# Performance work log

Measured on AMD Instinct MI355X. Metric: run time of the kernel, lower is better.

Reference implementation:

```python
import jax, jax.numpy as jnp
import numpy as np

T, B, E, H = 2048, 4, 1024, 16
D = E // H  # head_dim = 64
SCALING = D ** -0.5


def setup_inputs() -> dict:
    key = jax.random.key(0)
    ks = jax.random.split(key, 5)
    w_scale = (2.0 / (E + E)) ** 0.5  # xavier_uniform-ish std
    return {
        "query": jax.random.normal(ks[0], (T, B, E), dtype=jnp.float32),
        "q_weight": jax.random.normal(ks[1], (E, E), dtype=jnp.float32) * w_scale,
        "k_weight": jax.random.normal(ks[2], (E, E), dtype=jnp.float32) * w_scale,
        "v_weight": jax.random.normal(ks[3], (E, E), dtype=jnp.float32) * w_scale,
        "out_proj_weight": jax.random.normal(ks[4], (E, E), dtype=jnp.float32) * w_scale,
        "q_bias": jnp.zeros((E,), dtype=jnp.float32),
        "k_bias": jnp.zeros((E,), dtype=jnp.float32),
        "v_bias": jnp.zeros((E,), dtype=jnp.float32),
        "out_proj_bias": jnp.zeros((E,), dtype=jnp.float32),
    }


def reference(query, q_weight, k_weight, v_weight, out_proj_weight,
              q_bias, k_bias, v_bias, out_proj_bias):
    # Linear projections: y = x @ W.T + b  (torch F.linear convention)
    q = jnp.einsum('tbe,fe->tbf', query, q_weight) + q_bias
    k = jnp.einsum('tbe,fe->tbf', query, k_weight) + k_bias
    v = jnp.einsum('tbe,fe->tbf', query, v_weight) + v_bias
    # split heads: [T, B, H, D]
    q = q.reshape(T, B, H, D) * SCALING
    k = k.reshape(T, B, H, D)
    v = v.reshape(T, B, H, D)
    # attention scores [B, H, T, T] over keys s
    scores = jnp.einsum('tbhd,sbhd->bhts', q, k)
    attn = jax.nn.softmax(scores, axis=-1)
    # context [T, B, H, D] -> [T, B, E]
    ctx = jnp.einsum('bhts,sbhd->tbhd', attn, v).reshape(T, B, E)
    # output projection
    out = jnp.einsum('tbe,fe->tbf', ctx, out_proj_weight) + out_proj_bias
    return out
```

## Files before the change

kernel.cpp:

```cpp
#include <hip/hip_runtime.h>
#include <hip/hip_bf16.h>
#include <stdint.h>

#define T_   2048
#define B_   4
#define E_   1024
#define H_   16
#define D_   64
#define M_   8192
#define KDIM 1024

using bf16 = __hip_bfloat16;
typedef __attribute__((ext_vector_type(8)))  short bf16x8;
typedef __attribute__((ext_vector_type(4)))  float f32x4;
typedef __attribute__((ext_vector_type(16))) float f32x16;

#define QK_SCALE 0.180336880f

#if __has_builtin(__builtin_amdgcn_exp2f)
#define EXP2F(x) __builtin_amdgcn_exp2f(x)
#else
#define EXP2F(x) exp2f(x)
#endif

__device__ __forceinline__ void gload_lds16(const void* g, void* l) {
  __builtin_amdgcn_global_load_lds(
      (const __attribute__((address_space(1))) void*)g,
      (__attribute__((address_space(3))) void*)l, 16, 0, 0);
}

__device__ __forceinline__ uint32_t pack_bf16(float lo, float hi) {
  union { __hip_bfloat162 h2; uint32_t u; } cv;
  cv.h2 = __float22bfloat162_rn(float2{lo, hi});
  return cv.u;
}

__device__ __forceinline__ void plswap(uint32_t& a, uint32_t& b) {
#if __has_builtin(__builtin_amdgcn_permlane32_swap)
  typedef __attribute__((ext_vector_type(2))) unsigned int u32x2_t;
  u32x2_t r = __builtin_amdgcn_permlane32_swap(a, b, false, false);
  a = r[0]; b = r[1];
#else
  asm volatile("v_permlane32_swap_b32 %0, %1" : "+v"(a), "+v"(b));
#endif
}
__device__ __forceinline__ float comb_add32(float x) {
  union { float f; uint32_t u; } a, b; a.f = x; b.f = x;
  plswap(a.u, b.u);
  return a.f + b.f;
}

__global__ void k_cvt_all(const float* __restrict__ X,
                          const float* __restrict__ Wq, const float* __restrict__ Wk,
                          const float* __restrict__ Wv, const float* __restrict__ Wo,
                          bf16* __restrict__ Xb,
                          bf16* __restrict__ Wqb, bf16* __restrict__ Wkb,
                          bf16* __restrict__ Wvb, bf16* __restrict__ Wob) {
  int id = blockIdx.x;
  const float* src; bf16* dst; int base;
  if (id < 8192) { src = X; dst = Xb; base = id; }
  else {
    int w = (id - 8192) >> 10;
    base = (id - 8192) & 1023;
    src = (w == 0) ? Wq : (w == 1) ? Wk : (w == 2) ? Wv : Wo;
    dst = (w == 0) ? Wqb : (w == 1) ? Wkb : (w == 2) ? Wvb : Wob;
  }
  int i = base * 256 + threadIdx.x;
  float4 v = reinterpret_cast<const float4*>(src)[i];
  bf16* d = dst + (size_t)i * 4;
  d[0] = __float2bfloat16(v.x);
  d[1] = __float2bfloat16(v.y);
  d[2] = __float2bfloat16(v.z);
  d[3] = __float2bfloat16(v.w);
}

__device__ __forceinline__ void gemm_tile_body(
    const bf16* __restrict__ A, const bf16* __restrict__ Bw,
    int bm, int bn, bf16* sA, bf16* sB, f32x4 (&acc)[4][4])
{
  const int t    = threadIdx.x;
  const int wave = t >> 6;
  const int lane = t & 63;
  const int l15  = lane & 15, l4 = lane >> 4;
  const int wr = wave >> 1, wc = wave & 1;
  const int srow = t >> 3;
  const int sg   = t & 7;

  for (int k0 = 0; k0 < KDIM; k0 += 64) {
#pragma unroll
    for (int rd = 0; rd < 4; ++rd) {
      int row = rd * 32 + srow;
      const bf16* src = A + (size_t)(bm * 128 + row) * KDIM + k0 + ((sg ^ (row & 7)) * 8);
      gload_lds16(src, sA + rd * 2048 + wave * 512);
    }
#pragma unroll
    for (int rd = 0; rd < 4; ++rd) {
      int row = rd * 32 + srow;
      const bf16* src = Bw + (size_t)(bn * 128 + row) * KDIM + k0 + ((sg ^ (row & 7)) * 8);
      gload_lds16(src, sB + rd * 2048 + wave * 512);
    }
    __syncthreads();

#pragma unroll
    for (int kk = 0; kk < 2; ++kk) {
      bf16x8 af[4], bfr[4];
#pragma unroll
      for (int m = 0; m < 4; ++m) {
        int row = wr * 64 + m * 16 + l15;
        int ch  = (l4 + kk * 4) ^ (row & 7);
        af[m] = *(const bf16x8*)(sA + row * 64 + ch * 8);
      }
#pragma unroll
      for (int n = 0; n < 4; ++n) {
        int row = wc * 64 + n * 16 + l15;
        int ch  = (l4 + kk * 4) ^ (row & 7);
        bfr[n] = *(const bf16x8*)(sB + row * 64 + ch * 8);
      }
#pragma unroll
      for (int m = 0; m < 4; ++m)
#pragma unroll
        for (int n = 0; n < 4; ++n)
          acc[m][n] = __builtin_amdgcn_mfma_f32_16x16x32_bf16(af[m], bfr[n], acc[m][n], 0, 0, 0);
    }
    __syncthreads();
  }
}

__global__ __launch_bounds__(256, 3) void k_gemm_qkv(
    const bf16* __restrict__ A,
    const bf16* __restrict__ Wq, const bf16* __restrict__ Wk, const bf16* __restrict__ Wv,
    const float* __restrict__ bq, const float* __restrict__ bk, const float* __restrict__ bv,
    bf16* __restrict__ outQ)
{
  __shared__ bf16 sA[128 * 64];
  __shared__ bf16 sB[128 * 64];
  const int bid = blockIdx.x;
  const int xcd = bid & 7;
  const int l   = bid >> 3;
  const int g   = l / 24;
  const int w   = l % 24;
  const int bm  = g * 8 + (w & 7);
  const int bn  = xcd * 3 + (w >> 3);
  const int which = bn >> 3;
  const int bnn = bn & 7;
  const bf16* Bw = (which == 0) ? Wq : (which == 1) ? Wk : Wv;
  const float* bias = (which == 0) ? bq : (which == 1) ? bk : bv;
  const float scale = (which == 0) ? QK_SCALE : 1.0f;
  bf16* outb = outQ + (size_t)which * M_ * E_;

  f32x4 acc[4][4] = {};
  gemm_tile_body(A, Bw, bm, bnn, sA, sB, acc);

  const int lane = threadIdx.x & 63;
  const int l15 = lane & 15, l4 = lane >> 4;
  const int wave = threadIdx.x >> 6;
  const int wr = wave >> 1, wc = wave & 1;
#pragma unroll
  for (int m = 0; m < 4; ++m) {
#pragma unroll
    for (int n = 0; n < 4; ++n) {
      int gc = bnn * 128 + wc * 64 + n * 16 + l15;
      float bv_ = bias[gc];
#pragma unroll
      for (int r = 0; r < 4; ++r) {
        int gr = bm * 128 + wr * 64 + m * 16 + l4 * 4 + r;
        float v = (acc[m][n][r] + bv_) * scale;
        int tt = gr >> 2, bb = gr & 3;
        int hh = gc >> 6, dd = gc & 63;
        outb[(((size_t)(bb * H_ + hh)) * T_ + tt) * D_ + dd] = __float2bfloat16(v);
      }
    }
  }
}

__global__ __launch_bounds__(256, 3) void k_gemm_out(
    const bf16* __restrict__ A, const bf16* __restrict__ Bw,
    const float* __restrict__ bias, float* __restrict__ outf)
{
  __shared__ bf16 sA[128 * 64];
  __shared__ bf16 sB[128 * 64];
  const int bid = blockIdx.x;
  const int swz = (bid & 7) * 64 + (bid >> 3);
  const int bm = swz & 63;
  const int bn = swz >> 6;

  f32x4 acc[4][4] = {};
  gemm_tile_body(A, Bw, bm, bn, sA, sB, acc);

  const int lane = threadIdx.x & 63;
  const int l15 = lane & 15, l4 = lane >> 4;
  const int wave = threadIdx.x >> 6;
  const int wr = wave >> 1, wc = wave & 1;
#pragma unroll
  for (int m = 0; m < 4; ++m) {
#pragma unroll
    for (int n = 0; n < 4; ++n) {
      int gc = bn * 128 + wc * 64 + n * 16 + l15;
      float bv_ = bias[gc];
#pragma unroll
      for (int r = 0; r < 4; ++r) {
        int gr = bm * 128 + wr * 64 + m * 16 + l4 * 4 + r;
        outf[(size_t)gr * E_ + gc] = acc[m][n][r] + bv_;
      }
    }
  }
}

__global__ __launch_bounds__(256, 4) void k_attn5(
    const bf16* __restrict__ Qb, const bf16* __restrict__ Kb,
    const bf16* __restrict__ Vb, bf16* __restrict__ ctx)
{
  __shared__ bf16 sK [128 * 64];
  __shared__ bf16 sVT[2 * 64 * 64];

  const int t    = threadIdx.x;
  const int wave = t >> 6;
  const int lane = t & 63;
  const int l31  = lane & 31;
  const int h    = lane >> 5;

  const int bid = blockIdx.x;
  const int swz = (bid & 7) * 128 + (bid >> 3);
  const int bh  = swz >> 4;
  const int qt  = swz & 15;
  const int q0  = qt * 128;
  const size_t headoff = (size_t)bh * T_ * D_;

  const int qrow = q0 + wave * 32 + l31;
  bf16x8 qf[4];
#pragma unroll
  for (int kc = 0; kc < 4; ++kc)
    qf[kc] = *(const bf16x8*)(Qb + headoff + (size_t)qrow * 64 + kc * 16 + 8 * h);

  f32x16 acc0 = {}, acc1 = {};
  float lrun = 0.f;

  const int srow = t >> 3, sg = t & 7;
  const int vkey = (t >> 3) * 2, vd0 = (t & 7) * 8;

  int off_qk[4][2];
#pragma unroll
  for (int kc = 0; kc < 4; ++kc) {
    int slot = ((2 * kc + h) ^ (l31 & 7)) * 8;
    off_qk[kc][0] = l31 * 64 + slot;
    off_qk[kc][1] = (32 + l31) * 64 + slot;
  }
  int off_pv[4][2];
#pragma unroll
  for (int ks = 0; ks < 4; ++ks) {
    int d0 = l31, d1 = 32 + l31;
    off_pv[ks][0] = d0 * 64 + (((2 * ks + h) ^ (d0 & 7) ^ (d0 >> 3)) * 8);
    off_pv[ks][1] = d1 * 64 + (((2 * ks + h) ^ (d1 & 7) ^ (d1 >> 3)) * 8);
  }
  int off_vw[8];
#pragma unroll
  for (int j = 0; j < 8; ++j) {
    int d = vd0 + j;
    off_vw[j] = d * 64 + (((vkey >> 3) ^ (d & 7) ^ (d >> 3)) * 8) + (vkey & 7);
  }
  const int koff = srow * 64 + ((sg ^ (srow & 7)) * 8);

  for (int kt = 0; kt < T_ / 128; ++kt) {
    const bf16* ktile = Kb + headoff + (size_t)(kt * 128) * D_;
#pragma unroll
    for (int rd = 0; rd < 4; ++rd) {
      gload_lds16(ktile + (size_t)rd * 2048 + koff, sK + rd * 2048 + wave * 512);
    }
#pragma unroll
    for (int s = 0; s < 2; ++s) {
      const bf16* vtile = Vb + headoff + (size_t)(kt * 128 + s * 64) * D_;
      bf16x8 va = *(const bf16x8*)(vtile + (size_t)vkey * 64 + vd0);
      bf16x8 vb = *(const bf16x8*)(vtile + (size_t)(vkey + 1) * 64 + vd0);
#pragma unroll
      for (int j = 0; j < 8; ++j) {
        uint32_t pk = (uint32_t)(uint16_t)va[j] | ((uint32_t)(uint16_t)vb[j] << 16);
        *reinterpret_cast<uint32_t*>(sVT + s * 4096 + off_vw[j]) = pk;
      }
    }
    __syncthreads();

#pragma unroll
    for (int s = 0; s < 2; ++s) {
      f32x16 s0 = {}, s1 = {};
      __builtin_amdgcn_s_setprio(1);
#pragma unroll
      for (int kc = 0; kc < 4; ++kc) {
        bf16x8 a0 = *(const bf16x8*)(sK + s * 4096 + off_qk[kc][0]);
        bf16x8 a1 = *(const bf16x8*)(sK + s * 4096 + off_qk[kc][1]);
        s0 = __builtin_amdgcn_mfma_f32_32x32x16_bf16(a0, qf[kc], s0, 0, 0, 0);
        s1 = __builtin_amdgcn_mfma_f32_32x32x16_bf16(a1, qf[kc], s1, 0, 0, 0);
      }
      __builtin_amdgcn_s_setprio(0);

      float psum = 0.f;
#pragma unroll
      for (int r = 0; r < 16; ++r) { s0[r] = EXP2F(s0[r]); psum += s0[r]; }
#pragma unroll
      for (int r = 0; r < 16; ++r) { s1[r] = EXP2F(s1[r]); psum += s1[r]; }
      lrun += psum;

      uint32_t u[8][2];
#pragma unroll
      for (int g = 0; g < 4; ++g) {
        u[g][0]     = pack_bf16(s0[g * 4 + 0], s0[g * 4 + 1]);
        u[g][1]     = pack_bf16(s0[g * 4 + 2], s0[g * 4 + 3]);
        u[4 + g][0] = pack_bf16(s1[g * 4 + 0], s1[g * 4 + 1]);
        u[4 + g][1] = pack_bf16(s1[g * 4 + 2], s1[g * 4 + 3]);
      }

      bf16x8 pa[4];
#pragma unroll
      for (int ks = 0; ks < 4; ++ks) {
        uint32_t w0 = u[2 * ks][0], w2 = u[2 * ks + 1][0];
        uint32_t w1 = u[2 * ks][1], w3 = u[2 * ks + 1][1];
        plswap(w0, w2);
        plswap(w1, w3);
        union { uint32_t w[4]; bf16x8 v; } cv;
        cv.w[0] = w0; cv.w[1] = w1; cv.w[2] = w2; cv.w[3] = w3;
        pa[ks] = cv.v;
      }

      __builtin_amdgcn_s_setprio(1);
#pragma unroll
      for (int ks = 0; ks < 4; ++ks) {
        bf16x8 v0 = *(const bf16x8*)(sVT + s * 4096 + off_pv[ks][0]);
        bf16x8 v1 = *(const bf16x8*)(sVT + s * 4096 + off_pv[ks][1]);
        acc0 = __builtin_amdgcn_mfma_f32_32x32x16_bf16(v0, pa[ks], acc0, 0, 0, 0);
        acc1 = __builtin_amdgcn_mfma_f32_32x32x16_bf16(v1, pa[ks], acc1, 0, 0, 0);
      }
      __builtin_amdgcn_s_setprio(0);
    }
    __syncthreads();
  }

  float lt = comb_add32(lrun);
  float rinv = 1.0f / lt;
  const int b = bh >> 4, hh = bh & 15;
#pragma unroll
  for (int dt = 0; dt < 2; ++dt) {
#pragma unroll
    for (int g = 0; g < 4; ++g) {
      float e0 = (dt ? acc1[g * 4 + 0] : acc0[g * 4 + 0]) * rinv;
      float e1 = (dt ? acc1[g * 4 + 1] : acc0[g * 4 + 1]) * rinv;
      float e2 = (dt ? acc1[g * 4 + 2] : acc0[g * 4 + 2]) * rinv;
      float e3 = (dt ? acc1[g * 4 + 3] : acc0[g * 4 + 3]) * rinv;
      int dbase = dt * 32 + g * 8 + 4 * h;
      uint2 wv = { pack_bf16(e0, e1), pack_bf16(e2, e3) };
      *reinterpret_cast<uint2*>(ctx + ((size_t)qrow * B_ + b) * E_ + hh * 64 + dbase) = wv;
    }
  }
}

extern "C" void kernel_launch(void* const* d_in, const int* in_sizes, int n_in,
                              void* d_out, int out_size, void* d_ws, size_t ws_size,
                              hipStream_t stream) {
  const float* X  = (const float*)d_in[0];
  const float* Wq = (const float*)d_in[1];
  const float* Wk = (const float*)d_in[2];
  const float* Wv = (const float*)d_in[3];
  const float* Wo = (const float*)d_in[4];
  const float* bq = (const float*)d_in[5];
  const float* bk = (const float*)d_in[6];
  const float* bv = (const float*)d_in[7];
  const float* bo = (const float*)d_in[8];
  float* out = (float*)d_out;

  char* ws = (char*)d_ws;
  const size_t XB   = (size_t)M_ * E_ * 2;
  const size_t WB   = (size_t)E_ * E_ * 2;
  bf16* Xb  = (bf16*)(ws);
  bf16* Wqb = (bf16*)(ws + XB);
  bf16* Wkb = (bf16*)(ws + XB + WB);
  bf16* Wvb = (bf16*)(ws + XB + 2 * WB);
  bf16* Wob = (bf16*)(ws + XB + 3 * WB);
  bf16* Qb  = (bf16*)(ws + XB + 4 * WB);
  bf16* Kb  = (bf16*)(ws + 2 * XB + 4 * WB);
  bf16* Vb  = (bf16*)(ws + 3 * XB + 4 * WB);
  bf16* Cx  = Xb;

  k_cvt_all<<<12288, 256, 0, stream>>>(X, Wq, Wk, Wv, Wo, Xb, Wqb, Wkb, Wvb, Wob);

  k_gemm_qkv<<<1536, 256, 0, stream>>>(Xb, Wqb, Wkb, Wvb, bq, bk, bv, Qb);

  k_attn5<<<1024, 256, 0, stream>>>(Qb, Kb, Vb, Cx);

  k_gemm_out<<<512, 256, 0, stream>>>(Cx, Wob, bo, out);
}
```

Measured before the change: 184.0 us.

## Shrink attention blocks to 2 waves with 64-key tiles and MFMA row sums

```diff
diff --git a/kernel.cpp b/kernel.cpp
--- a/kernel.cpp
+++ b/kernel.cpp
@@ -43,11 +43,6 @@
 #else
   asm volatile("v_permlane32_swap_b32 %0, %1" : "+v"(a), "+v"(b));
 #endif
-}
-__device__ __forceinline__ float comb_add32(float x) {
-  union { float f; uint32_t u; } a, b; a.f = x; b.f = x;
-  plswap(a.u, b.u);
-  return a.f + b.f;
 }
 
 __global__ void k_cvt_all(const float* __restrict__ X,
@@ -206,12 +201,12 @@
   }
 }
 
-__global__ __launch_bounds__(256, 4) void k_attn5(
+__global__ __launch_bounds__(128, 4) void k_attn7(
     const bf16* __restrict__ Qb, const bf16* __restrict__ Kb,
     const bf16* __restrict__ Vb, bf16* __restrict__ ctx)
 {
-  __shared__ bf16 sK [128 * 64];
-  __shared__ bf16 sVT[2 * 64 * 64];
+  __shared__ bf16 sK [64 * 64];
+  __shared__ bf16 sVT[64 * 64];
 
   const int t    = threadIdx.x;
   const int wave = t >> 6;
@@ -220,10 +215,10 @@
   const int h    = lane >> 5;
 
   const int bid = blockIdx.x;
-  const int swz = (bid & 7) * 128 + (bid >> 3);
-  const int bh  = swz >> 4;
-  const int qt  = swz & 15;
-  const int q0  = qt * 128;
+  const int swz = (bid & 7) * 256 + (bid >> 3);
+  const int bh  = swz >> 5;
+  const int qt  = swz & 31;
+  const int q0  = qt * 64;
   const size_t headoff = (size_t)bh * T_ * D_;
 
   const int qrow = q0 + wave * 32 + l31;
@@ -232,11 +227,17 @@
   for (int kc = 0; kc < 4; ++kc)
     qf[kc] = *(const bf16x8*)(Qb + headoff + (size_t)qrow * 64 + kc * 16 + 8 * h);
 
+  bf16x8 ones;
+#pragma unroll
+  for (int j = 0; j < 8; ++j) ones[j] = (short)0x3F80;
+
   f32x16 acc0 = {}, acc1 = {};
-  float lrun = 0.f;
-
-  const int srow = t >> 3, sg = t & 7;
-  const int vkey = (t >> 3) * 2, vd0 = (t & 7) * 8;
+  f32x16 acc2 = {};
+
+  const int srow = t >> 3;
+  const int sg   = t & 7;
+  const int vkey = (t >> 3) * 4;
+  const int vd0  = (t & 7) * 8;
 
   int off_qk[4][2];
 #pragma unroll
@@ -260,81 +261,77 @@
   }
   const int koff = srow * 64 + ((sg ^ (srow & 7)) * 8);
 
-  for (int kt = 0; kt < T_ / 128; ++kt) {
-    const bf16* ktile = Kb + headoff + (size_t)(kt * 128) * D_;
+  for (int kt = 0; kt < T_ / 64; ++kt) {
+    const bf16* ktile = Kb + headoff + (size_t)(kt * 64) * D_;
 #pragma unroll
     for (int rd = 0; rd < 4; ++rd) {
-      gload_lds16(ktile + (size_t)rd * 2048 + koff, sK + rd * 2048 + wave * 512);
-    }
-#pragma unroll
-    for (int s = 0; s < 2; ++s) {
-      const bf16* vtile = Vb + headoff + (size_t)(kt * 128 + s * 64) * D_;
-      bf16x8 va = *(const bf16x8*)(vtile + (size_t)vkey * 64 + vd0);
-      bf16x8 vb = *(const bf16x8*)(vtile + (size_t)(vkey + 1) * 64 + vd0);
-#pragma unroll
-      for (int j = 0; j < 8; ++j) {
-        uint32_t pk = (uint32_t)(uint16_t)va[j] | ((uint32_t)(uint16_t)vb[j] << 16);
-        *reinterpret_cast<uint32_t*>(sVT + s * 4096 + off_vw[j]) = pk;
-      }
+      gload_lds16(ktile + (size_t)rd * 1024 + koff, sK + rd * 1024 + wave * 512);
+    }
+    const bf16* vtile = Vb + headoff + (size_t)(kt * 64) * D_;
+    bf16x8 va = *(const bf16x8*)(vtile + (size_t)(vkey + 0) * 64 + vd0);
+    bf16x8 vb = *(const bf16x8*)(vtile + (size_t)(vkey + 1) * 64 + vd0);
+    bf16x8 vc = *(const bf16x8*)(vtile + (size_t)(vkey + 2) * 64 + vd0);
+    bf16x8 vd = *(const bf16x8*)(vtile + (size_t)(vkey + 3) * 64 + vd0);
+#pragma unroll
+    for (int j = 0; j < 8; ++j) {
+      uint32_t p01 = (uint32_t)(uint16_t)va[j] | ((uint32_t)(uint16_t)vb[j] << 16);
+      uint32_t p23 = (uint32_t)(uint16_t)vc[j] | ((uint32_t)(uint16_t)vd[j] << 16);
+      *reinterpret_cast<uint32_t*>(sVT + off_vw[j])     = p01;
+      *reinterpret_cast<uint32_t*>(sVT + off_vw[j] + 2) = p23;
     }
     __syncthreads();
 
-#pragma unroll
-    for (int s = 0; s < 2; ++s) {
-      f32x16 s0 = {}, s1 = {};
-      __builtin_amdgcn_s_setprio(1);
-#pragma unroll
-      for (int kc = 0; kc < 4; ++kc) {
-        bf16x8 a0 = *(const bf16x8*)(sK + s * 4096 + off_qk[kc][0]);
-        bf16x8 a1 = *(const bf16x8*)(sK + s * 4096 + off_qk[kc][1]);
-        s0 = __builtin_amdgcn_mfma_f32_32x32x16_bf16(a0, qf[kc], s0, 0, 0, 0);
-        s1 = __builtin_amdgcn_mfma_f32_32x32x16_bf16(a1, qf[kc], s1, 0, 0, 0);
-      }
-      __builtin_amdgcn_s_setprio(0);
-
-      float psum = 0.f;
-#pragma unroll
-      for (int r = 0; r < 16; ++r) { s0[r] = EXP2F(s0[r]); psum += s0[r]; }
-#pragma unroll
-      for (int r = 0; r < 16; ++r) { s1[r] = EXP2F(s1[r]); psum += s1[r]; }
-      lrun += psum;
-
-      uint32_t u[8][2];
-#pragma unroll
-      for (int g = 0; g < 4; ++g) {
-        u[g][0]     = pack_bf16(s0[g * 4 + 0], s0[g * 4 + 1]);
-        u[g][1]     = pack_bf16(s0[g * 4 + 2], s0[g * 4 + 3]);
-        u[4 + g][0] = pack_bf16(s1[g * 4 + 0], s1[g * 4 + 1]);
-        u[4 + g][1] = pack_bf16(s1[g * 4 + 2], s1[g * 4 + 3]);
-      }
-
-      bf16x8 pa[4];
-#pragma unroll
-      for (int ks = 0; ks < 4; ++ks) {
-        uint32_t w0 = u[2 * ks][0], w2 = u[2 * ks + 1][0];
-        uint32_t w1 = u[2 * ks][1], w3 = u[2 * ks + 1][1];
-        plswap(w0, w2);
-        plswap(w1, w3);
-        union { uint32_t w[4]; bf16x8 v; } cv;
-        cv.w[0] = w0; cv.w[1] = w1; cv.w[2] = w2; cv.w[3] = w3;
-        pa[ks] = cv.v;
-      }
-
-      __builtin_amdgcn_s_setprio(1);
-#pragma unroll
-      for (int ks = 0; ks < 4; ++ks) {
-        bf16x8 v0 = *(const bf16x8*)(sVT + s * 4096 + off_pv[ks][0]);
-        bf16x8 v1 = *(const bf16x8*)(sVT + s * 4096 + off_pv[ks][1]);
-        acc0 = __builtin_amdgcn_mfma_f32_32x32x16_bf16(v0, pa[ks], acc0, 0, 0, 0);
-        acc1 = __builtin_amdgcn_mfma_f32_32x32x16_bf16(v1, pa[ks], acc1, 0, 0, 0);
-      }
-      __builtin_amdgcn_s_setprio(0);
-    }
+    f32x16 s0 = {}, s1 = {};
+    __builtin_amdgcn_s_setprio(1);
+#pragma unroll
+    for (int kc = 0; kc < 4; ++kc) {
+      bf16x8 a0 = *(const bf16x8*)(sK + off_qk[kc][0]);
+      bf16x8 a1 = *(const bf16x8*)(sK + off_qk[kc][1]);
+      s0 = __builtin_amdgcn_mfma_f32_32x32x16_bf16(a0, qf[kc], s0, 0, 0, 0);
+      s1 = __builtin_amdgcn_mfma_f32_32x32x16_bf16(a1, qf[kc], s1, 0, 0, 0);
+    }
+    __builtin_amdgcn_s_setprio(0);
+
+#pragma unroll
+    for (int r = 0; r < 16; ++r) s0[r] = EXP2F(s0[r]);
+#pragma unroll
+    for (int r = 0; r < 16; ++r) s1[r] = EXP2F(s1[r]);
+
+    uint32_t u[8][2];
+#pragma unroll
+    for (int g = 0; g < 4; ++g) {
+      u[g][0]     = pack_bf16(s0[g * 4 + 0], s0[g * 4 + 1]);
+      u[g][1]     = pack_bf16(s0[g * 4 + 2], s0[g * 4 + 3]);
+      u[4 + g][0] = pack_bf16(s1[g * 4 + 0], s1[g * 4 + 1]);
+      u[4 + g][1] = pack_bf16(s1[g * 4 + 2], s1[g * 4 + 3]);
+    }
+
+    bf16x8 pa[4];
+#pragma unroll
+    for (int ks = 0; ks < 4; ++ks) {
+      uint32_t w0 = u[2 * ks][0], w2 = u[2 * ks + 1][0];
+      uint32_t w1 = u[2 * ks][1], w3 = u[2 * ks + 1][1];
+      plswap(w0, w2);
+      plswap(w1, w3);
+      union { uint32_t w[4]; bf16x8 v; } cv;
+      cv.w[0] = w0; cv.w[1] = w1; cv.w[2] = w2; cv.w[3] = w3;
+      pa[ks] = cv.v;
+    }
+
+    __builtin_amdgcn_s_setprio(1);
+#pragma unroll
+    for (int ks = 0; ks < 4; ++ks) {
+      bf16x8 v0 = *(const bf16x8*)(sVT + off_pv[ks][0]);
+      bf16x8 v1 = *(const bf16x8*)(sVT + off_pv[ks][1]);
+      acc0 = __builtin_amdgcn_mfma_f32_32x32x16_bf16(v0, pa[ks], acc0, 0, 0, 0);
+      acc1 = __builtin_amdgcn_mfma_f32_32x32x16_bf16(v1, pa[ks], acc1, 0, 0, 0);
+      acc2 = __builtin_amdgcn_mfma_f32_32x32x16_bf16(ones, pa[ks], acc2, 0, 0, 0);
+    }
+    __builtin_amdgcn_s_setprio(0);
     __syncthreads();
   }
 
-  float lt = comb_add32(lrun);
-  float rinv = 1.0f / lt;
+  float rinv = 1.0f / acc2[0];
   const int b = bh >> 4, hh = bh & 15;
 #pragma unroll
   for (int dt = 0; dt < 2; ++dt) {
@@ -382,7 +379,7 @@
 
   k_gemm_qkv<<<1536, 256, 0, stream>>>(Xb, Wqb, Wkb, Wvb, bq, bk, bv, Qb);
 
-  k_attn5<<<1024, 256, 0, stream>>>(Qb, Kb, Vb, Cx);
+  k_attn7<<<2048, 128, 0, stream>>>(Qb, Kb, Vb, Cx);
 
   k_gemm_out<<<512, 256, 0, stream>>>(Cx, Wob, bo, out);
 }
```

After: 219.6 us. 1.19x slower.
